# Performance work log

Measured on AMD Instinct MI355X. Metric: run time of the kernel, lower is better.

Reference implementation:

```python
import jax, jax.numpy as jnp
import numpy as np

B, T, N, E = 4, 8, 512, 8192
CIN, H, HEADS = 64, 128, 4


def setup_inputs() -> dict:
    key = jax.random.key(0)
    ks = jax.random.split(key, 8)
    G = B * T
    s = 0.05
    return {
        "x": jax.random.normal(ks[0], (G, N, CIN), jnp.float32),
        "edge_index": jax.random.randint(ks[1], (G, 2, E), 0, N, dtype=jnp.int64),
        "W1": jax.random.normal(ks[2], (CIN, H), jnp.float32) * s,
        "b1": jnp.zeros((H,), jnp.float32),
        "W2": jax.random.normal(ks[3], (H, H), jnp.float32) * s,
        "b2": jnp.zeros((H,), jnp.float32),
        "in_proj_w": jax.random.normal(ks[4], (3 * H, H), jnp.float32) * s,
        "in_proj_b": jnp.zeros((3 * H,), jnp.float32),
        "out_proj_w": jax.random.normal(ks[5], (H, H), jnp.float32) * s,
        "out_proj_b": jnp.zeros((H,), jnp.float32),
    }


def gcn_layer(x, src, dst, W, b, num_nodes):
    # PyG GCNConv: add self-loops, sym-normalize deg^-1/2[src]*deg^-1/2[dst]
    xl = x @ W                                            # [GN, H]
    deg = jax.ops.segment_sum(jnp.ones_like(dst, dtype=xl.dtype), dst,
                              num_segments=num_nodes) + 1.0  # +1 self-loop
    dinv = jax.lax.rsqrt(deg)
    norm = dinv[src] * dinv[dst]                          # [Etot]
    agg = jax.ops.segment_sum(xl[src] * norm[:, None], dst, num_segments=num_nodes)
    agg = agg + xl * (dinv * dinv)[:, None]               # self-loop term
    return agg + b


def reference(x, edge_index, W1, b1, W2, b2, in_proj_w, in_proj_b, out_proj_w, out_proj_b):
    G, n, cin = x.shape
    GN = G * n
    offs = (jnp.arange(G, dtype=edge_index.dtype) * n)[:, None]  # disjoint union
    src = (edge_index[:, 0, :] + offs).reshape(-1)
    dst = (edge_index[:, 1, :] + offs).reshape(-1)
    xf = x.reshape(GN, cin)
    h = gcn_layer(xf, src, dst, W1, b1, GN)
    h = gcn_layer(h, src, dst, W2, b2, GN)
    hc = h.shape[-1]
    h = h.reshape(B, T * n, hc)                           # [B, S, H]
    # torch.nn.MultiheadAttention with packed qkv in_proj
    qkv = h @ in_proj_w.T + in_proj_b
    q, k, v = jnp.split(qkv, 3, axis=-1)
    hd = hc // HEADS
    def sh(t):
        return t.reshape(B, -1, HEADS, hd).transpose(0, 2, 1, 3)  # [B,h,S,d]
    q, k, v = sh(q), sh(k), sh(v)
    att = jax.nn.softmax(jnp.einsum('bhqd,bhkd->bhqk', q, k) / jnp.sqrt(jnp.float32(hd)), axis=-1)
    o = jnp.einsum('bhqk,bhkd->bhqd', att, v).transpose(0, 2, 1, 3).reshape(B, -1, hc)
    return o @ out_proj_w.T + out_proj_b
```

## Files before the change

### kernel.cpp

```cpp
#include <hip/hip_runtime.h>
#include <hip/hip_bf16.h>

#define G     32
#define NPG   512
#define EPG   8192
#define GN    16384
#define ETOT  (G*EPG)
#define CIN   64
#define H     128
#define NB    4
#define S     4096
#define HEADS 4
#define HD    32
#define QKV   384

typedef __attribute__((ext_vector_type(8))) short short8;
typedef __attribute__((ext_vector_type(4))) float floatx4;

__device__ __forceinline__ float bf16_to_f32(unsigned short u) {
    unsigned int x = ((unsigned int)u) << 16;
    return __uint_as_float(x);
}
__device__ __forceinline__ unsigned short f32_to_bf16(float f) {
    __hip_bfloat16 h = (__hip_bfloat16)f;
    return *(unsigned short*)&h;
}
__device__ __forceinline__ float ldf(const void* p, long i, int f32) {
    return f32 ? ((const float*)p)[i] : bf16_to_f32(((const unsigned short*)p)[i]);
}

__global__ void detect_kernel(const unsigned short* __restrict__ xraw,
                              const int* __restrict__ eiraw, int* __restrict__ flags) {
    __shared__ float smax[256];
    __shared__ int   sor[256];
    int t = threadIdx.x;
    float m = 0.f;
    for (int i = t; i < 4096; i += 256)
        m = fmaxf(m, fabsf(bf16_to_f32(xraw[i])));
    int orv = 0;
    for (int i = t; i < 2048; i += 256)
        orv |= eiraw[2 * i + 1];
    smax[t] = m; sor[t] = orv;
    __syncthreads();
    for (int off = 128; off > 0; off >>= 1) {
        if (t < off) {
            smax[t] = fmaxf(smax[t], smax[t + off]);
            sor[t] |= sor[t + off];
        }
        __syncthreads();
    }
    if (t == 0) {
        flags[0] = (smax[0] > 1000.f) ? 1 : 0;
        flags[1] = (sor[0] == 0) ? 1 : 0;
    }
}

#define XN   (GN*CIN)
#define E1   (XN + H*CIN)
#define E2   (E1 + H*H)
#define E3   (E2 + QKV*H)
#define E4   (E3 + H*H)
#define E5   (E4 + H)
#define E6   (E5 + H)
#define E7   (E6 + QKV)
#define CTOT (E7 + H)
__global__ void conv_all_kernel(const void* x_raw, const void* W1_raw, const void* b1_raw,
                                const void* W2_raw, const void* b2_raw, const void* Wq_raw,
                                const void* bq_raw, const void* Wo_raw, const void* bo_raw,
                                unsigned short* __restrict__ xb,
                                unsigned short* __restrict__ W1T,
                                unsigned short* __restrict__ W2T,
                                unsigned short* __restrict__ Wqb,
                                unsigned short* __restrict__ Wob,
                                float* __restrict__ b1f, float* __restrict__ b2f,
                                float* __restrict__ bqf, float* __restrict__ bof,
                                const float* __restrict__ dinv,
                                const int* __restrict__ flags) {
    int i = blockIdx.x * blockDim.x + threadIdx.x;
    if (i >= CTOT) return;
    int f32 = flags[0];
    if (i < XN) {
        xb[i] = f32_to_bf16(ldf(x_raw, i, f32) * dinv[i >> 6]);
    } else if (i < E1) {
        int j = i - XN, c = j / CIN, r = j - c * CIN;
        W1T[j] = f32_to_bf16(ldf(W1_raw, (long)r * H + c, f32));
    } else if (i < E2) {
        int j = i - E1, c = j >> 7, r = j & 127;
        W2T[j] = f32_to_bf16(ldf(W2_raw, (long)r * H + c, f32));
    } else if (i < E3) {
        int j = i - E2;
        Wqb[j] = f32_to_bf16(ldf(Wq_raw, j, f32));
    } else if (i < E4) {
        int j = i - E3;
        Wob[j] = f32_to_bf16(ldf(Wo_raw, j, f32));
    } else if (i < E5) { b1f[i - E4] = ldf(b1_raw, i - E4, f32); }
    else if (i < E6) { b2f[i - E5] = ldf(b2_raw, i - E5, f32); }
    else if (i < E7) { bqf[i - E6] = ldf(bq_raw, i - E6, f32); }
    else             { bof[i - E7] = ldf(bo_raw, i - E7, f32); }
}

__global__ void edges_count_kernel(const int* __restrict__ ei, int* __restrict__ srcA,
                                   int* __restrict__ dstA, int* __restrict__ cnt,
                                   const int* __restrict__ flags) {
    int t = blockIdx.x * blockDim.x + threadIdx.x;
    if (t >= ETOT) return;
    int g = t >> 13, e = t & (EPG - 1);
    int sh = flags[1];
    long long si = ((long long)(g * 2 + 0) * EPG + e) << sh;
    long long di = ((long long)(g * 2 + 1) * EPG + e) << sh;
    int s = g * NPG + ei[si];
    int d = g * NPG + ei[di];
    srcA[t] = s;
    dstA[t] = d;
    atomicAdd(&cnt[d], 1);
}

__global__ void scan_kernel(const int* __restrict__ cnt, int* __restrict__ row_start,
                            int* __restrict__ fill_pos, float* __restrict__ dinv) {
    __shared__ int tmp[NPG];
    int g = blockIdx.x, t = threadIdx.x;
    int c = cnt[g * NPG + t];
    tmp[t] = c;
    __syncthreads();
    for (int off = 1; off < NPG; off <<= 1) {
        int v = (t >= off) ? tmp[t - off] : 0;
        __syncthreads();
        tmp[t] += v;
        __syncthreads();
    }
    int excl = tmp[t] - c;
    int rs = g * EPG + excl;
    row_start[g * NPG + t] = rs;
    fill_pos[g * NPG + t]  = rs;
    dinv[g * NPG + t] = 1.0f / sqrtf((float)c + 1.0f);
}

__global__ void fill_kernel(const int* __restrict__ srcA, const int* __restrict__ dstA,
                            int* __restrict__ fill_pos, int* __restrict__ csr_src) {
    int t = blockIdx.x * blockDim.x + threadIdx.x;
    if (t >= ETOT) return;
    int pos = atomicAdd(&fill_pos[dstA[t]], 1);
    csr_src[pos] = srcA[t];
}

__global__ void agg64_kernel(const unsigned short* __restrict__ xb,
                             const int* __restrict__ row_start, const int* __restrict__ cnt,
                             const int* __restrict__ csr_src, const float* __restrict__ dinv,
                             unsigned short* __restrict__ z) {
    int i = blockIdx.x;
    int c = threadIdx.x;
    float acc = bf16_to_f32(xb[(size_t)i * CIN + c]);
    int rs = row_start[i], n = cnt[i];
    int p = 0;
    for (; p + 4 <= n; p += 4) {
        int s0 = csr_src[rs + p + 0];
        int s1 = csr_src[rs + p + 1];
        int s2 = csr_src[rs + p + 2];
        int s3 = csr_src[rs + p + 3];
        float a0 = bf16_to_f32(xb[(size_t)s0 * CIN + c]);
        float a1 = bf16_to_f32(xb[(size_t)s1 * CIN + c]);
        float a2 = bf16_to_f32(xb[(size_t)s2 * CIN + c]);
        float a3 = bf16_to_f32(xb[(size_t)s3 * CIN + c]);
        acc += (a0 + a1) + (a2 + a3);
    }
    for (; p < n; p++)
        acc += bf16_to_f32(xb[(size_t)csr_src[rs + p] * CIN + c]);
    z[(size_t)i * CIN + c] = f32_to_bf16(acc * dinv[i]);
}

template<int KD>
__global__ __launch_bounds__(256) void mm_bias_kernel(const unsigned short* __restrict__ A,
        const unsigned short* __restrict__ B, const float* __restrict__ bias,
        unsigned short* __restrict__ Y) {
    int tid = threadIdx.x, wave = tid >> 6, lane = tid & 63, m = lane & 15, quad = lane >> 4;
    int row0 = blockIdx.x * 64 + wave * 16;
    floatx4 acc[8] = {};
    for (int kc = 0; kc < KD; kc += 32) {
        short8 af = *(const short8*)&A[(size_t)(row0 + m) * KD + kc + quad * 8];
#pragma unroll
        for (int t = 0; t < 8; t++) {
            short8 bf = *(const short8*)&B[(size_t)(t * 16 + m) * KD + kc + quad * 8];
            acc[t] = __builtin_amdgcn_mfma_f32_16x16x32_bf16(af, bf, acc[t], 0, 0, 0);
        }
    }
    int rbase = row0 + quad * 4;
#pragma unroll
    for (int t = 0; t < 8; t++) {
        int col = t * 16 + m;
        float bj = bias[col];
#pragma unroll
        for (int r = 0; r < 4; r++)
            Y[(size_t)(rbase + r) * H + col] = f32_to_bf16(acc[t][r] + bj);
    }
}

template<int KD>
__global__ __launch_bounds__(256) void mm_gcn_kernel(const unsigned short* __restrict__ A,
        const unsigned short* __restrict__ B, const float* __restrict__ dinv,
        unsigned short* __restrict__ Y) {
    int tid = threadIdx.x, wave = tid >> 6, lane = tid & 63, m = lane & 15, quad = lane >> 4;
    int row0 = blockIdx.x * 64 + wave * 16;
    floatx4 acc[8] = {};
    for (int kc = 0; kc < KD; kc += 32) {
        short8 af = *(const short8*)&A[(size_t)(row0 + m) * KD + kc + quad * 8];
#pragma unroll
        for (int t = 0; t < 8; t++) {
            short8 bf = *(const short8*)&B[(size_t)(t * 16 + m) * KD + kc + quad * 8];
            acc[t] = __builtin_amdgcn_mfma_f32_16x16x32_bf16(af, bf, acc[t], 0, 0, 0);
        }
    }
    int rbase = row0 + quad * 4;
    float4 dv4 = *(const float4*)&dinv[rbase];
    float dv[4] = {dv4.x, dv4.y, dv4.z, dv4.w};
#pragma unroll
    for (int t = 0; t < 8; t++) {
        int col = t * 16 + m;
#pragma unroll
        for (int r = 0; r < 4; r++)
            Y[(size_t)(rbase + r) * H + col] = f32_to_bf16(acc[t][r] * dv[r]);
    }
}

__global__ void agg_kernel(const unsigned short* __restrict__ y,
                           const int* __restrict__ row_start, const int* __restrict__ cnt,
                           const int* __restrict__ csr_src, const float* __restrict__ dinv,
                           const float* __restrict__ bias, unsigned short* __restrict__ hout) {
    int i = blockIdx.x;
    int c = threadIdx.x;
    float acc = bf16_to_f32(y[(size_t)i * H + c]);
    int rs = row_start[i], n = cnt[i];
    int p = 0;
    for (; p + 4 <= n; p += 4) {
        int s0 = csr_src[rs + p + 0];
        int s1 = csr_src[rs + p + 1];
        int s2 = csr_src[rs + p + 2];
        int s3 = csr_src[rs + p + 3];
        float a0 = bf16_to_f32(y[(size_t)s0 * H + c]);
        float a1 = bf16_to_f32(y[(size_t)s1 * H + c]);
        float a2 = bf16_to_f32(y[(size_t)s2 * H + c]);
        float a3 = bf16_to_f32(y[(size_t)s3 * H + c]);
        acc += (a0 + a1) + (a2 + a3);
    }
    for (; p < n; p++)
        acc += bf16_to_f32(y[(size_t)csr_src[rs + p] * H + c]);
    hout[(size_t)i * H + c] = f32_to_bf16(acc * dinv[i] + bias[c]);
}

__global__ __launch_bounds__(256) void mmqkv_kernel(const unsigned short* __restrict__ A,
        const unsigned short* __restrict__ B, const float* __restrict__ bias,
        unsigned short* __restrict__ Qx, unsigned short* __restrict__ Kx,
        unsigned short* __restrict__ Vtx) {
    int tid = threadIdx.x, wave = tid >> 6, lane = tid & 63, m = lane & 15, quad = lane >> 4;
    int row0 = blockIdx.x * 64 + wave * 16;
    floatx4 acc[24] = {};
    for (int kc = 0; kc < H; kc += 32) {
        short8 af = *(const short8*)&A[(size_t)(row0 + m) * H + kc + quad * 8];
#pragma unroll
        for (int t = 0; t < 24; t++) {
            short8 bf = *(const short8*)&B[(size_t)(t * 16 + m) * H + kc + quad * 8];
            acc[t] = __builtin_amdgcn_mfma_f32_16x16x32_bf16(af, bf, acc[t], 0, 0, 0);
        }
    }
    int rbase = row0 + quad * 4;
    int b = rbase >> 12, s0 = rbase & (S - 1);
#pragma unroll
    for (int t = 0; t < 24; t++) {
        int j = t * 16 + m;
        float bj = bias[j];
        int jj = j & 127, head = jj >> 5, hd = jj & 31;
        int bh = b * HEADS + head;
        if (t < 8) {
#pragma unroll
            for (int r = 0; r < 4; r++)
                Qx[((size_t)bh * S + s0 + r) * HD + hd] =
                    f32_to_bf16((acc[t][r] + bj) *
                                (0.17677669529663687f * 1.4426950408889634f));
        } else if (t < 16) {
#pragma unroll
            for (int r = 0; r < 4; r++)
                Kx[((size_t)bh * S + s0 + r) * HD + hd] = f32_to_bf16(acc[t][r] + bj);
        } else {
#pragma unroll
            for (int r = 0; r < 4; r++)
                Vtx[((size_t)bh * HD + hd) * S + s0 + r] = f32_to_bf16(acc[t][r] + bj);
        }
    }
}

__global__ __launch_bounds__(256) void attn7_kernel(
        const unsigned short* __restrict__ Qx, const unsigned short* __restrict__ Kx,
        const unsigned short* __restrict__ Vtx, unsigned short* __restrict__ Ob) {
    int tid = threadIdx.x, wave = tid >> 6, lane = tid & 63;
    int m = lane & 15, quad = lane >> 4;

    int n = blockIdx.x;
    int id = (n & 7) * 32 + (n >> 3);
    int tile = id & 15, bh = id >> 4;

    const unsigned short* Qb  = Qx  + (size_t)bh * S * HD;
    const unsigned short* Kb  = Kx  + (size_t)bh * S * HD;
    const unsigned short* Vtb = Vtx + (size_t)bh * HD * S;

    int q0 = tile * 256 + wave * 64;
    short8 q[4];
#pragma unroll
    for (int t = 0; t < 4; t++)
        q[t] = *(const short8*)&Qb[(size_t)(q0 + t * 16 + m) * HD + quad * 8];

    floatx4 o0[4] = {}, o1[4] = {}, l[4] = {};

    short8 ones = {16256, 16256, 16256, 16256, 16256, 16256, 16256, 16256};
    union PW { unsigned int u[4]; short8 s8; };

    short8 kf0 = *(const short8*)&Kb[(size_t)m * HD + quad * 8];
    short8 kf1 = *(const short8*)&Kb[(size_t)(m + 16) * HD + quad * 8];
    short8 vc0 = *(const short8*)&Vtb[(size_t)m * S + quad * 8];
    short8 vc1 = *(const short8*)&Vtb[(size_t)(m + 16) * S + quad * 8];

    for (int i = 0; i < S / 32; i++) {
        floatx4 z = {};
        floatx4 t0[4], t1[4];
#pragma unroll
        for (int t = 0; t < 4; t++) {
            t0[t] = __builtin_amdgcn_mfma_f32_16x16x32_bf16(kf0, q[t], z, 0, 0, 0);
            t1[t] = __builtin_amdgcn_mfma_f32_16x16x32_bf16(kf1, q[t], z, 0, 0, 0);
        }
        int ktn = ((i + 1) * 32) & (S - 1);
        kf0 = *(const short8*)&Kb[(size_t)(ktn + m) * HD + quad * 8];
        kf1 = *(const short8*)&Kb[(size_t)(ktn + m + 16) * HD + quad * 8];

        PW pw[4];
#pragma unroll
        for (int t = 0; t < 4; t++) {
            float e0 = __builtin_amdgcn_exp2f(t0[t][0]);
            float e1 = __builtin_amdgcn_exp2f(t0[t][1]);
            float e2 = __builtin_amdgcn_exp2f(t0[t][2]);
            float e3 = __builtin_amdgcn_exp2f(t0[t][3]);
            float e4 = __builtin_amdgcn_exp2f(t1[t][0]);
            float e5 = __builtin_amdgcn_exp2f(t1[t][1]);
            float e6 = __builtin_amdgcn_exp2f(t1[t][2]);
            float e7 = __builtin_amdgcn_exp2f(t1[t][3]);
            unsigned int w0, w1, w2, w3;
            asm("v_cvt_pk_bf16_f32 %0, %1, %2" : "=v"(w0) : "v"(e0), "v"(e1));
            asm("v_cvt_pk_bf16_f32 %0, %1, %2" : "=v"(w1) : "v"(e2), "v"(e3));
            asm("v_cvt_pk_bf16_f32 %0, %1, %2" : "=v"(w2) : "v"(e4), "v"(e5));
            asm("v_cvt_pk_bf16_f32 %0, %1, %2" : "=v"(w3) : "v"(e6), "v"(e7));
            asm("v_permlane32_swap_b32 %0, %1" : "+v"(w0), "+v"(w2));
            asm("v_permlane32_swap_b32 %0, %1" : "+v"(w1), "+v"(w3));
            asm("v_permlane16_swap_b32 %0, %1" : "+v"(w0), "+v"(w2));
            asm("v_permlane16_swap_b32 %0, %1" : "+v"(w1), "+v"(w3));
            pw[t].u[0] = w0; pw[t].u[1] = w1; pw[t].u[2] = w2; pw[t].u[3] = w3;
        }

#pragma unroll
        for (int t = 0; t < 4; t++) {
            o0[t] = __builtin_amdgcn_mfma_f32_16x16x32_bf16(pw[t].s8, vc0, o0[t], 0, 0, 0);
            o1[t] = __builtin_amdgcn_mfma_f32_16x16x32_bf16(pw[t].s8, vc1, o1[t], 0, 0, 0);
            l[t]  = __builtin_amdgcn_mfma_f32_16x16x32_bf16(pw[t].s8, ones, l[t], 0, 0, 0);
        }
        vc0 = *(const short8*)&Vtb[(size_t)m * S + ktn + quad * 8];
        vc1 = *(const short8*)&Vtb[(size_t)(m + 16) * S + ktn + quad * 8];
    }

    int batch = bh >> 2, head = bh & 3;
    int col = head * HD + m;
#pragma unroll
    for (int t = 0; t < 4; t++) {
        int grow = batch * S + q0 + t * 16 + quad * 4;
#pragma unroll
        for (int r = 0; r < 4; r++) {
            float inv = 1.f / l[t][r];
            Ob[(size_t)(grow + r) * H + col]      = f32_to_bf16(o0[t][r] * inv);
            Ob[(size_t)(grow + r) * H + col + 16] = f32_to_bf16(o1[t][r] * inv);
        }
    }
}

__global__ __launch_bounds__(256) void mmout_kernel(const unsigned short* __restrict__ A,
        const unsigned short* __restrict__ B, const float* __restrict__ bias,
        void* __restrict__ out, const int* __restrict__ flags) {
    int tid = threadIdx.x, wave = tid >> 6, lane = tid & 63, m = lane & 15, quad = lane >> 4;
    int row0 = blockIdx.x * 64 + wave * 16;
    floatx4 acc[8] = {};
    for (int kc = 0; kc < H; kc += 32) {
        short8 af = *(const short8*)&A[(size_t)(row0 + m) * H + kc + quad * 8];
#pragma unroll
        for (int t = 0; t < 8; t++) {
            short8 bf = *(const short8*)&B[(size_t)(t * 16 + m) * H + kc + quad * 8];
            acc[t] = __builtin_amdgcn_mfma_f32_16x16x32_bf16(af, bf, acc[t], 0, 0, 0);
        }
    }
    int rbase = row0 + quad * 4;
    int f32o = flags[0];
#pragma unroll
    for (int t = 0; t < 8; t++) {
        int col = t * 16 + m;
        float bj = bias[col];
#pragma unroll
        for (int r = 0; r < 4; r++) {
            float v = acc[t][r] + bj;
            if (f32o) ((float*)out)[(size_t)(rbase + r) * H + col] = v;
            else ((unsigned short*)out)[(size_t)(rbase + r) * H + col] = f32_to_bf16(v);
        }
    }
}

extern "C" void kernel_launch(void* const* d_in, const int* in_sizes, int n_in,
                              void* d_out, int out_size, void* d_ws, size_t ws_size,
                              hipStream_t stream) {
    const void* x_raw    = d_in[0];
    const int*  ei_raw   = (const int*)d_in[1];
    const void* W1_raw   = d_in[2];
    const void* b1_raw   = d_in[3];
    const void* W2_raw   = d_in[4];
    const void* b2_raw   = d_in[5];
    const void* Wq_raw   = d_in[6];
    const void* bq_raw   = d_in[7];
    const void* Wo_raw   = d_in[8];
    const void* bo_raw   = d_in[9];

    char* ws = (char*)d_ws;
    size_t o = 0;
    auto alloc = [&](size_t bytes) { void* p = ws + o; o += (bytes + 1023) & ~1023ull; return p; };

    int*   flags     = (int*)  alloc(1024);
    int*   cnt       = (int*)  alloc((size_t)GN * 4);
    int*   row_start = (int*)  alloc((size_t)GN * 4);
    int*   fill_pos  = (int*)  alloc((size_t)GN * 4);
    float* dinv      = (float*)alloc((size_t)GN * 4);
    int*   srcA      = (int*)  alloc((size_t)ETOT * 4);
    int*   dstA      = (int*)  alloc((size_t)ETOT * 4);
    int*   csr_src   = (int*)  alloc((size_t)ETOT * 4);
    unsigned short* xb   = (unsigned short*)alloc((size_t)GN * CIN * 2);
    unsigned short* zb   = (unsigned short*)alloc((size_t)GN * CIN * 2);
    unsigned short* W1T  = (unsigned short*)alloc((size_t)H * CIN * 2);
    unsigned short* W2T  = (unsigned short*)alloc((size_t)H * H * 2);
    unsigned short* Wqb  = (unsigned short*)alloc((size_t)QKV * H * 2);
    unsigned short* Wob  = (unsigned short*)alloc((size_t)H * H * 2);
    float* b1f = (float*)alloc(H * 4);
    float* b2f = (float*)alloc(H * 4);
    float* bqf = (float*)alloc(QKV * 4);
    float* bof = (float*)alloc(H * 4);
    unsigned short* y_bf = (unsigned short*)alloc((size_t)GN * H * 2);
    unsigned short* h_bf = (unsigned short*)alloc((size_t)GN * H * 2);
    unsigned short* Qx   = (unsigned short*)alloc((size_t)16 * S * HD * 2);
    unsigned short* Kx   = (unsigned short*)alloc((size_t)16 * S * HD * 2);
    unsigned short* Vtx  = (unsigned short*)alloc((size_t)16 * S * HD * 2);
    unsigned short* Obf  = y_bf;

    detect_kernel<<<1, 256, 0, stream>>>((const unsigned short*)x_raw, ei_raw, flags);

    hipMemsetAsync(cnt, 0, (size_t)GN * 4, stream);
    edges_count_kernel<<<ETOT / 256, 256, 0, stream>>>(ei_raw, srcA, dstA, cnt, flags);
    scan_kernel<<<G, NPG, 0, stream>>>(cnt, row_start, fill_pos, dinv);

    conv_all_kernel<<<(CTOT + 255) / 256, 256, 0, stream>>>(
        x_raw, W1_raw, b1_raw, W2_raw, b2_raw, Wq_raw, bq_raw, Wo_raw, bo_raw,
        xb, W1T, W2T, Wqb, Wob, b1f, b2f, bqf, bof, dinv, flags);

    fill_kernel<<<ETOT / 256, 256, 0, stream>>>(srcA, dstA, fill_pos, csr_src);

    agg64_kernel<<<GN, CIN, 0, stream>>>(xb, row_start, cnt, csr_src, dinv, zb);
    mm_bias_kernel<CIN><<<GN / 64, 256, 0, stream>>>(zb, W1T, b1f, h_bf);
    mm_gcn_kernel<H><<<GN / 64, 256, 0, stream>>>(h_bf, W2T, dinv, y_bf);
    agg_kernel<<<GN, H, 0, stream>>>(y_bf, row_start, cnt, csr_src, dinv, b2f, h_bf);

    mmqkv_kernel<<<GN / 64, 256, 0, stream>>>(h_bf, Wqb, bqf, Qx, Kx, Vtx);
    attn7_kernel<<<dim3(256), 256, 0, stream>>>(Qx, Kx, Vtx, Obf);
    mmout_kernel<<<GN / 64, 256, 0, stream>>>(Obf, Wob, bof, d_out, flags);
}
```

Before: 258.3 us.

## Fuse CSR build into one per-graph kernel, fuse GCN matmuls, coalesce V transpose

Replaces the edge-count, scan and fill kernels plus the memset with a single per-graph kernel that uses shared-memory atomics for the counts, the scan and the fill positions, which removes the global srcA/dstA arrays and several launches. It fuses the two GCN matmuls into one kernel that passes the intermediate tile through LDS instead of global memory. It also stages the V output through LDS so the transposed V stores are written as packed, coalesced chunks. The CSR kernel runs on only 32 blocks, which may limit parallelism, and the CSR fill order still depends on atomic ordering.

```diff
diff --git a/kernel.cpp b/kernel.cpp
--- a/kernel.cpp
+++ b/kernel.cpp
@@ -52,6 +52,43 @@
     if (t == 0) {
         flags[0] = (smax[0] > 1000.f) ? 1 : 0;
         flags[1] = (sor[0] == 0) ? 1 : 0;
+    }
+}
+
+__global__ __launch_bounds__(NPG) void csr_kernel(const int* __restrict__ ei,
+        const int* __restrict__ flags, int* __restrict__ cnt_g,
+        int* __restrict__ row_start_g, float* __restrict__ dinv_g,
+        int* __restrict__ csr_src) {
+    __shared__ int cs[NPG], ctmp[NPG], fpos[NPG];
+    int g = blockIdx.x, t = threadIdx.x;
+    int sh = flags[1];
+    cs[t] = 0;
+    __syncthreads();
+    const size_t sbase = ((size_t)(g * 2 + 0) * EPG) << sh;
+    const size_t dbase = ((size_t)(g * 2 + 1) * EPG) << sh;
+    for (int e = t; e < EPG; e += NPG)
+        atomicAdd(&cs[ei[dbase + ((size_t)e << sh)]], 1);
+    __syncthreads();
+    int c = cs[t];
+    ctmp[t] = c;
+    __syncthreads();
+    for (int off = 1; off < NPG; off <<= 1) {
+        int v = (t >= off) ? ctmp[t - off] : 0;
+        __syncthreads();
+        ctmp[t] += v;
+        __syncthreads();
+    }
+    int rs = g * EPG + ctmp[t] - c;
+    fpos[t] = rs;
+    cnt_g[g * NPG + t] = c;
+    row_start_g[g * NPG + t] = rs;
+    dinv_g[g * NPG + t] = 1.0f / sqrtf((float)c + 1.0f);
+    __syncthreads();
+    for (int e = t; e < EPG; e += NPG) {
+        int s = ei[sbase + ((size_t)e << sh)];
+        int d = ei[dbase + ((size_t)e << sh)];
+        int pos = atomicAdd(&fpos[d], 1);
+        csr_src[pos] = g * NPG + s;
     }
 }
 
@@ -99,50 +136,6 @@
     else             { bof[i - E7] = ldf(bo_raw, i - E7, f32); }
 }
 
-__global__ void edges_count_kernel(const int* __restrict__ ei, int* __restrict__ srcA,
-                                   int* __restrict__ dstA, int* __restrict__ cnt,
-                                   const int* __restrict__ flags) {
-    int t = blockIdx.x * blockDim.x + threadIdx.x;
-    if (t >= ETOT) return;
-    int g = t >> 13, e = t & (EPG - 1);
-    int sh = flags[1];
-    long long si = ((long long)(g * 2 + 0) * EPG + e) << sh;
-    long long di = ((long long)(g * 2 + 1) * EPG + e) << sh;
-    int s = g * NPG + ei[si];
-    int d = g * NPG + ei[di];
-    srcA[t] = s;
-    dstA[t] = d;
-    atomicAdd(&cnt[d], 1);
-}
-
-__global__ void scan_kernel(const int* __restrict__ cnt, int* __restrict__ row_start,
-                            int* __restrict__ fill_pos, float* __restrict__ dinv) {
-    __shared__ int tmp[NPG];
-    int g = blockIdx.x, t = threadIdx.x;
-    int c = cnt[g * NPG + t];
-    tmp[t] = c;
-    __syncthreads();
-    for (int off = 1; off < NPG; off <<= 1) {
-        int v = (t >= off) ? tmp[t - off] : 0;
-        __syncthreads();
-        tmp[t] += v;
-        __syncthreads();
-    }
-    int excl = tmp[t] - c;
-    int rs = g * EPG + excl;
-    row_start[g * NPG + t] = rs;
-    fill_pos[g * NPG + t]  = rs;
-    dinv[g * NPG + t] = 1.0f / sqrtf((float)c + 1.0f);
-}
-
-__global__ void fill_kernel(const int* __restrict__ srcA, const int* __restrict__ dstA,
-                            int* __restrict__ fill_pos, int* __restrict__ csr_src) {
-    int t = blockIdx.x * blockDim.x + threadIdx.x;
-    if (t >= ETOT) return;
-    int pos = atomicAdd(&fill_pos[dstA[t]], 1);
-    csr_src[pos] = srcA[t];
-}
-
 __global__ void agg64_kernel(const unsigned short* __restrict__ xb,
                              const int* __restrict__ row_start, const int* __restrict__ cnt,
                              const int* __restrict__ csr_src, const float* __restrict__ dinv,
@@ -168,45 +161,40 @@
     z[(size_t)i * CIN + c] = f32_to_bf16(acc * dinv[i]);
 }
 
-template<int KD>
-__global__ __launch_bounds__(256) void mm_bias_kernel(const unsigned short* __restrict__ A,
-        const unsigned short* __restrict__ B, const float* __restrict__ bias,
-        unsigned short* __restrict__ Y) {
+#define HPAD 136
+__global__ __launch_bounds__(256) void gcn12_kernel(
+        const unsigned short* __restrict__ Z, const unsigned short* __restrict__ W1T,
+        const float* __restrict__ b1, const unsigned short* __restrict__ W2T,
+        const float* __restrict__ dinv, unsigned short* __restrict__ Y) {
+    __shared__ unsigned short hl[64][HPAD];
     int tid = threadIdx.x, wave = tid >> 6, lane = tid & 63, m = lane & 15, quad = lane >> 4;
     int row0 = blockIdx.x * 64 + wave * 16;
+    int lrow0 = wave * 16;
     floatx4 acc[8] = {};
-    for (int kc = 0; kc < KD; kc += 32) {
-        short8 af = *(const short8*)&A[(size_t)(row0 + m) * KD + kc + quad * 8];
+    for (int kc = 0; kc < CIN; kc += 32) {
+        short8 af = *(const short8*)&Z[(size_t)(row0 + m) * CIN + kc + quad * 8];
 #pragma unroll
         for (int t = 0; t < 8; t++) {
-            short8 bf = *(const short8*)&B[(size_t)(t * 16 + m) * KD + kc + quad * 8];
+            short8 bf = *(const short8*)&W1T[(size_t)(t * 16 + m) * CIN + kc + quad * 8];
             acc[t] = __builtin_amdgcn_mfma_f32_16x16x32_bf16(af, bf, acc[t], 0, 0, 0);
         }
     }
-    int rbase = row0 + quad * 4;
 #pragma unroll
     for (int t = 0; t < 8; t++) {
         int col = t * 16 + m;
-        float bj = bias[col];
+        float bj = b1[col];
 #pragma unroll
         for (int r = 0; r < 4; r++)
-            Y[(size_t)(rbase + r) * H + col] = f32_to_bf16(acc[t][r] + bj);
-    }
-}
-
-template<int KD>
-__global__ __launch_bounds__(256) void mm_gcn_kernel(const unsigned short* __restrict__ A,
-        const unsigned short* __restrict__ B, const float* __restrict__ dinv,
-        unsigned short* __restrict__ Y) {
-    int tid = threadIdx.x, wave = tid >> 6, lane = tid & 63, m = lane & 15, quad = lane >> 4;
-    int row0 = blockIdx.x * 64 + wave * 16;
-    floatx4 acc[8] = {};
-    for (int kc = 0; kc < KD; kc += 32) {
-        short8 af = *(const short8*)&A[(size_t)(row0 + m) * KD + kc + quad * 8];
+            hl[lrow0 + quad * 4 + r][col] = f32_to_bf16(acc[t][r] + bj);
+    }
+    asm volatile("s_waitcnt lgkmcnt(0)" ::: "memory");
+    floatx4 acc2[8] = {};
+    for (int kc = 0; kc < H; kc += 32) {
+        short8 af = *(const short8*)&hl[lrow0 + m][kc + quad * 8];
 #pragma unroll
         for (int t = 0; t < 8; t++) {
-            short8 bf = *(const short8*)&B[(size_t)(t * 16 + m) * KD + kc + quad * 8];
-            acc[t] = __builtin_amdgcn_mfma_f32_16x16x32_bf16(af, bf, acc[t], 0, 0, 0);
+            short8 bf = *(const short8*)&W2T[(size_t)(t * 16 + m) * H + kc + quad * 8];
+            acc2[t] = __builtin_amdgcn_mfma_f32_16x16x32_bf16(af, bf, acc2[t], 0, 0, 0);
         }
     }
     int rbase = row0 + quad * 4;
@@ -217,7 +205,7 @@
         int col = t * 16 + m;
 #pragma unroll
         for (int r = 0; r < 4; r++)
-            Y[(size_t)(rbase + r) * H + col] = f32_to_bf16(acc[t][r] * dv[r]);
+            Y[(size_t)(rbase + r) * H + col] = f32_to_bf16(acc2[t][r] * dv[r]);
     }
 }
 
@@ -250,6 +238,7 @@
         const unsigned short* __restrict__ B, const float* __restrict__ bias,
         unsigned short* __restrict__ Qx, unsigned short* __restrict__ Kx,
         unsigned short* __restrict__ Vtx) {
+    __shared__ unsigned short vbuf[4][2][16][20];
     int tid = threadIdx.x, wave = tid >> 6, lane = tid & 63, m = lane & 15, quad = lane >> 4;
     int row0 = blockIdx.x * 64 + wave * 16;
     floatx4 acc[24] = {};
@@ -263,26 +252,40 @@
     }
     int rbase = row0 + quad * 4;
     int b = rbase >> 12, s0 = rbase & (S - 1);
+    int s0t = row0 & (S - 1);
+    int hdl = lane >> 2, sg = lane & 3;
 #pragma unroll
     for (int t = 0; t < 24; t++) {
         int j = t * 16 + m;
         float bj = bias[j];
-        int jj = j & 127, head = jj >> 5, hd = jj & 31;
-        int bh = b * HEADS + head;
         if (t < 8) {
+            int head = j >> 5, hd = j & 31;
+            int bh = b * HEADS + head;
 #pragma unroll
             for (int r = 0; r < 4; r++)
                 Qx[((size_t)bh * S + s0 + r) * HD + hd] =
                     f32_to_bf16((acc[t][r] + bj) *
                                 (0.17677669529663687f * 1.4426950408889634f));
         } else if (t < 16) {
+            int jj = j & 127, head = jj >> 5, hd = jj & 31;
+            int bh = b * HEADS + head;
 #pragma unroll
             for (int r = 0; r < 4; r++)
                 Kx[((size_t)bh * S + s0 + r) * HD + hd] = f32_to_bf16(acc[t][r] + bj);
         } else {
-#pragma unroll
-            for (int r = 0; r < 4; r++)
-                Vtx[((size_t)bh * HD + hd) * S + s0 + r] = f32_to_bf16(acc[t][r] + bj);
+            int t2 = t - 16;
+            int head = t2 >> 1, hdb = (t2 & 1) * 16;
+            int bh = b * HEADS + head;
+            float v0 = acc[t][0] + bj, v1 = acc[t][1] + bj;
+            float v2 = acc[t][2] + bj, v3 = acc[t][3] + bj;
+            unsigned int d0, d1;
+            asm("v_cvt_pk_bf16_f32 %0, %1, %2" : "=v"(d0) : "v"(v0), "v"(v1));
+            asm("v_cvt_pk_bf16_f32 %0, %1, %2" : "=v"(d1) : "v"(v2), "v"(v3));
+            uint2 wv; wv.x = d0; wv.y = d1;
+            *(uint2*)&vbuf[wave][t2 & 1][m][quad * 4] = wv;
+            asm volatile("s_waitcnt lgkmcnt(0)" ::: "memory");
+            uint2 rv = *(const uint2*)&vbuf[wave][t2 & 1][hdl][sg * 4];
+            *(uint2*)&Vtx[((size_t)bh * HD + hdb + hdl) * S + s0t + sg * 4] = rv;
         }
     }
 }
@@ -426,10 +429,7 @@
     int*   flags     = (int*)  alloc(1024);
     int*   cnt       = (int*)  alloc((size_t)GN * 4);
     int*   row_start = (int*)  alloc((size_t)GN * 4);
-    int*   fill_pos  = (int*)  alloc((size_t)GN * 4);
     float* dinv      = (float*)alloc((size_t)GN * 4);
-    int*   srcA      = (int*)  alloc((size_t)ETOT * 4);
-    int*   dstA      = (int*)  alloc((size_t)ETOT * 4);
     int*   csr_src   = (int*)  alloc((size_t)ETOT * 4);
     unsigned short* xb   = (unsigned short*)alloc((size_t)GN * CIN * 2);
     unsigned short* zb   = (unsigned short*)alloc((size_t)GN * CIN * 2);
@@ -450,19 +450,14 @@
 
     detect_kernel<<<1, 256, 0, stream>>>((const unsigned short*)x_raw, ei_raw, flags);
 
-    hipMemsetAsync(cnt, 0, (size_t)GN * 4, stream);
-    edges_count_kernel<<<ETOT / 256, 256, 0, stream>>>(ei_raw, srcA, dstA, cnt, flags);
-    scan_kernel<<<G, NPG, 0, stream>>>(cnt, row_start, fill_pos, dinv);
+    csr_kernel<<<G, NPG, 0, stream>>>(ei_raw, flags, cnt, row_start, dinv, csr_src);
 
     conv_all_kernel<<<(CTOT + 255) / 256, 256, 0, stream>>>(
         x_raw, W1_raw, b1_raw, W2_raw, b2_raw, Wq_raw, bq_raw, Wo_raw, bo_raw,
         xb, W1T, W2T, Wqb, Wob, b1f, b2f, bqf, bof, dinv, flags);
 
-    fill_kernel<<<ETOT / 256, 256, 0, stream>>>(srcA, dstA, fill_pos, csr_src);
-
     agg64_kernel<<<GN, CIN, 0, stream>>>(xb, row_start, cnt, csr_src, dinv, zb);
-    mm_bias_kernel<CIN><<<GN / 64, 256, 0, stream>>>(zb, W1T, b1f, h_bf);
-    mm_gcn_kernel<H><<<GN / 64, 256, 0, stream>>>(h_bf, W2T, dinv, y_bf);
+    gcn12_kernel<<<GN / 64, 256, 0, stream>>>(zb, W1T, b1f, W2T, dinv, y_bf);
     agg_kernel<<<GN, H, 0, stream>>>(y_bf, row_start, cnt, csr_src, dinv, b2f, h_bf);
 
     mmqkv_kernel<<<GN / 64, 256, 0, stream>>>(h_bf, Wqb, bqf, Qx, Kx, Vtx);
```

Measured after the change: 249.9 us. 1.03x faster.
